# Kernel optimization log

Hardware: AMD Instinct MI355X
Metric: run time of the kernel (lower is better)

The kernel has to match this reference:

```python
import jax, jax.numpy as jnp
import numpy as np

B, SQ, SKV, D, H = 2, 2048, 2048, 1024, 16
HD = D // H  # 64
ROPE_BASE = 10000.0


def setup_inputs() -> dict:
    key = jax.random.key(0)
    ks = jax.random.split(key, 6)
    s = 1.0 / np.sqrt(D)  # keep activations well-scaled
    return {
        "x_q": jax.random.normal(ks[0], (B, SQ, D), jnp.float32),
        "x_kv": jax.random.normal(ks[1], (B, SKV, D), jnp.float32),
        "wq": jax.random.normal(ks[2], (D, D), jnp.float32) * s,
        "bq": jnp.zeros((D,), jnp.float32),
        "wk": jax.random.normal(ks[3], (D, D), jnp.float32) * s,
        "bk": jnp.zeros((D,), jnp.float32),
        "wv": jax.random.normal(ks[4], (D, D), jnp.float32) * s,
        "bv": jnp.zeros((D,), jnp.float32),
        "wo": jax.random.normal(ks[5], (D, D), jnp.float32) * s,
        "bo": jnp.zeros((D,), jnp.float32),
    }


def _rope_interleaved(x):
    # x: [B, S, H, HD]; sequential positions starting at 0 (GPT-NeoX style)
    s, hd = x.shape[1], x.shape[-1]
    dim = hd // 2
    freqs = jnp.exp(-jnp.arange(dim, dtype=x.dtype) * jnp.log(jnp.asarray(ROPE_BASE, x.dtype)) / dim)
    ang = jnp.arange(s, dtype=x.dtype)[:, None] * freqs[None, :]  # [S, dim]
    cos = jnp.cos(ang)[None, :, None, :]
    sin = jnp.sin(ang)[None, :, None, :]
    xe, xo = x[..., ::2], x[..., 1::2]
    re = xe * cos - xo * sin
    ro = xe * sin + xo * cos
    return jnp.stack([re, ro], axis=-1).reshape(x.shape)


def reference(x_q, x_kv, wq, bq, wk, bk, wv, bv, wo, bo):
    b, sq, _ = x_q.shape
    skv = x_kv.shape[1]
    q = (jnp.einsum("bsd,ed->bse", x_q, wq) + bq).reshape(b, sq, H, HD)
    k = (jnp.einsum("bsd,ed->bse", x_kv, wk) + bk).reshape(b, skv, H, HD)
    v = (jnp.einsum("bsd,ed->bse", x_kv, wv) + bv).reshape(b, skv, H, HD)
    q = _rope_interleaved(q)
    k = _rope_interleaved(k)
    scores = jnp.einsum("bqhd,bkhd->bhqk", q, k) / jnp.sqrt(jnp.asarray(HD, q.dtype))
    attn = jax.nn.softmax(scores, axis=-1)
    ctx = jnp.einsum("bhqk,bkhd->bqhd", attn, v).reshape(b, sq, D)
    return jnp.einsum("bsd,ed->bse", ctx, wo) + bo
```

## Files before the change

### kernel.cpp

```cpp
#include <hip/hip_runtime.h>
#include <cstdint>

typedef __attribute__((ext_vector_type(8))) short bf16x8;
typedef __attribute__((ext_vector_type(4))) float f32x4;
typedef __attribute__((ext_vector_type(4))) unsigned int u32x4;

#define DEV static __device__ __forceinline__

DEV unsigned short f2bf(float f) {
  unsigned int u = __builtin_bit_cast(unsigned int, f);
  u += 0x7FFFu + ((u >> 16) & 1u);
  return (unsigned short)(u >> 16);
}
#if __has_builtin(__builtin_amdgcn_cvt_pk_bf16_f32)
DEV unsigned int pkbf(float a, float b) {
  auto v = __builtin_amdgcn_cvt_pk_bf16_f32(a, b);
  return __builtin_bit_cast(unsigned int, v);
}
#else
DEV unsigned int pkbf(float a, float b) {
  return (unsigned int)f2bf(a) | ((unsigned int)f2bf(b) << 16);
}
#endif
#if __has_builtin(__builtin_amdgcn_exp2f)
#define EXP2(x) __builtin_amdgcn_exp2f(x)
#else
#define EXP2(x) exp2f(x)
#endif
DEV float bfl(unsigned int u) { return __builtin_bit_cast(float, u << 16); }
DEV float bfh(unsigned int u) { return __builtin_bit_cast(float, u & 0xFFFF0000u); }

DEV void async_copy16(const unsigned short* g, unsigned short* l) {
  __builtin_amdgcn_global_load_lds(
      (const __attribute__((address_space(1))) unsigned int*)(uintptr_t)g,
      (__attribute__((address_space(3))) unsigned int*)(uintptr_t)l,
      16, 0, 0);
}

#if __has_builtin(__builtin_amdgcn_permlane32_swap) && \
    __has_builtin(__builtin_amdgcn_permlane16_swap)
DEV void pswap(unsigned a, unsigned b, unsigned& w0, unsigned& w2, int lane) {
  (void)lane;
  auto pq = __builtin_amdgcn_permlane32_swap((int)a, (int)b, false, false);
  auto wz = __builtin_amdgcn_permlane16_swap(pq[0], pq[1], false, false);
  w0 = (unsigned)wz[0];
  w2 = (unsigned)wz[1];
}
#else
DEV void pswap(unsigned a, unsigned b, unsigned& w0, unsigned& w2, int lane) {
  int q = lane >> 4, l = lane & 15;
  int src0 = ((q & 1) << 5) + l;
  int a0 = __shfl((int)a, src0), b0 = __shfl((int)b, src0);
  int a2 = __shfl((int)a, src0 + 16), b2 = __shfl((int)b, src0 + 16);
  w0 = (unsigned)(q < 2 ? a0 : b0);
  w2 = (unsigned)(q < 2 ? a2 : b2);
}
#endif

__global__ __launch_bounds__(256) void cvt8(
    const float* __restrict__ w0, const float* __restrict__ w1,
    const float* __restrict__ w2, const float* __restrict__ w3,
    const float* __restrict__ x0, const float* __restrict__ x1,
    unsigned short* __restrict__ wsb, unsigned short* __restrict__ xb)
{
  int id = blockIdx.x * 256 + threadIdx.x;
  const float* src;
  unsigned short* dp;
  int off;
  if (id < (1 << 20)) {
    int m = id >> 18;
    off = (id & 0x3FFFF) << 2;
    src = m == 0 ? w0 : m == 1 ? w1 : m == 2 ? w2 : w3;
    dp = wsb + (((size_t)m) << 20) + off;
  } else {
    int id2 = id - (1 << 20);
    int m = id2 >> 20;
    off = (id2 & 0xFFFFF) << 2;
    src = m ? x1 : x0;
    dp = xb + (((size_t)m) << 22) + off;
  }
  float4 v = *(const float4*)(src + off);
  uint2 o;
  o.x = pkbf(v.x, v.y);
  o.y = pkbf(v.z, v.w);
  *(uint2*)dp = o;
}

__global__ __launch_bounds__(256) void gemm_qkv_bf(
    const unsigned short* __restrict__ xqb,
    const unsigned short* __restrict__ xkvb,
    const unsigned short* __restrict__ wbase,
    const float* __restrict__ bq, const float* __restrict__ bk,
    const float* __restrict__ bv,
    unsigned short* __restrict__ outq, unsigned short* __restrict__ outk,
    unsigned short* __restrict__ outvT)
{
  constexpr int K = 1024;
  __shared__ unsigned short As[128 * 32];
  __shared__ unsigned short Bs[128 * 32];
  const int z = blockIdx.z;
  const unsigned short* X = (z == 0) ? xqb : xkvb;
  const unsigned short* Wb = wbase + (((size_t)z) << 20);
  const float* bias = (z == 0) ? bq : (z == 1) ? bk : bv;

  const int tid = threadIdx.x;
  const int mBase = blockIdx.y * 128, nBase = blockIdx.x * 128;
  const int wave = tid >> 6, lane = tid & 63;
  const int quad = lane >> 4, l16 = lane & 15;
  const int wm = (wave >> 1) << 6, wn = (wave & 1) << 6;

  f32x4 acc[4][4] = {};

  for (int k0 = 0; k0 < K; k0 += 32) {
#pragma unroll
    for (int i = 0; i < 2; ++i) {
      int e = i * 2048 + tid * 8;
      int row = e >> 5, col = e & 31;
      async_copy16(X + (size_t)(mBase + row) * K + (k0 + col), &As[e]);
      async_copy16(Wb + (size_t)(nBase + row) * K + (k0 + col), &Bs[e]);
    }
    __syncthreads();
    bf16x8 af[4], bff[4];
#pragma unroll
    for (int t = 0; t < 4; ++t) {
      af[t]  = *(const bf16x8*)&As[(wm + t * 16 + l16) * 32 + quad * 8];
      bff[t] = *(const bf16x8*)&Bs[(wn + t * 16 + l16) * 32 + quad * 8];
    }
#pragma unroll
    for (int mt = 0; mt < 4; ++mt)
#pragma unroll
      for (int nt = 0; nt < 4; ++nt)
        acc[mt][nt] = __builtin_amdgcn_mfma_f32_16x16x32_bf16(af[mt], bff[nt], acc[mt][nt], 0, 0, 0);
    __syncthreads();
  }

  if (z < 2) {
    unsigned short* out = z ? outk : outq;
    const float qs = z ? 1.0f : 0.18033688011112042f;
    const int sBlk = (mBase & 2047) + wm + quad * 4;
#pragma unroll
    for (int nt = 0; nt < 4; ++nt) {
      int n = nBase + wn + nt * 16 + l16;
      float bv2 = bias[n];
      int h = n >> 6, hd = n & 63;
      int i = hd >> 1;
      int parity = n & 1;
      float f = exp2f(-(float)i * 0.4152410118609203f);
      float sf, cf;
      sincosf(f, &sf, &cf);
#pragma unroll
      for (int mt = 0; mt < 4; ++mt) {
        float ang = (float)(sBlk + mt * 16) * f;
        float s, c;
        sincosf(ang, &s, &c);
#pragma unroll
        for (int j = 0; j < 4; ++j) {
          float v = acc[mt][nt][j] + bv2;
          float pv = __shfl_xor(v, 1);
          float ce = c * qs;
          float se = (parity ? s : -s) * qs;
          float outv = v * ce + pv * se;
          int m = mBase + wm + mt * 16 + quad * 4 + j;
          int b = m >> 11, sv = m & 2047;
          out[(((size_t)(b * 16 + h) * 2048 + sv) << 6) + hd] = f2bf(outv);
          float c2 = c * cf - s * sf;
          s = s * cf + c * sf;
          c = c2;
        }
      }
    }
  } else {
#pragma unroll
    for (int nt = 0; nt < 4; ++nt) {
      int n = nBase + wn + nt * 16 + l16;
      float bv2 = bias[n];
      int h = n >> 6, hd = n & 63;
#pragma unroll
      for (int mt = 0; mt < 4; ++mt) {
        int m0 = mBase + wm + mt * 16 + quad * 4;
        int b = m0 >> 11, s = m0 & 2047;
        uint2 o;
        o.x = pkbf(acc[mt][nt][0] + bv2, acc[mt][nt][1] + bv2);
        o.y = pkbf(acc[mt][nt][2] + bv2, acc[mt][nt][3] + bv2);
        *(uint2*)&outvT[(((size_t)(b * 16 + h) * 64 + hd) << 11) + s] = o;
      }
    }
  }
}

__global__ __launch_bounds__(256) void attn_v7(
    const unsigned short* __restrict__ Qg,
    const unsigned short* __restrict__ Kg,
    const unsigned short* __restrict__ VT,
    unsigned short* __restrict__ Opart,
    float* __restrict__ lbuf)
{
  __shared__ unsigned short Ks[2][64 * 64];
  __shared__ unsigned short Vs[2][64 * 64];
  const int tid = threadIdx.x, wave = tid >> 6, lane = tid & 63;
  const int quad = lane >> 4, l16 = lane & 15;
  const int bh = blockIdx.x & 31;
  const int qt = (blockIdx.x >> 5) & 15;
  const int kvs = blockIdx.x >> 9;
  const int q0 = qt * 128 + wave * 32;
  const unsigned short* Qb = Qg + ((size_t)bh << 17);
  const unsigned short* Kb = Kg + ((size_t)bh << 17);
  const unsigned short* Vb = VT + ((size_t)bh << 17);

  const int L0 = tid, L1 = 256 + tid;
  const int r0 = L0 >> 3, r1 = L1 >> 3;
  const int c0 = ((L0 & 7) ^ (r0 & 7)) << 3;
  const int c1 = ((L1 & 7) ^ (r1 & 7)) << 3;

  bf16x8 qf[2][2];
#pragma unroll
  for (int mq = 0; mq < 2; ++mq)
#pragma unroll
    for (int kd = 0; kd < 2; ++kd)
      qf[mq][kd] = *(const bf16x8*)(Qb + (size_t)(q0 + mq * 16 + l16) * 64 + kd * 32 + quad * 8);

  f32x4 oacc[4][2] = {};
  float lacc[2] = { 0.f, 0.f };

  const int kvbeg = kvs << 10;
  const int swz = l16 & 7;

  {
    const int kv0 = kvbeg;
    async_copy16(Kb + (size_t)(kv0 + r0) * 64 + c0, &Ks[0][L0 * 8]);
    async_copy16(Kb + (size_t)(kv0 + r1) * 64 + c1, &Ks[0][L1 * 8]);
    async_copy16(Vb + (size_t)r0 * 2048 + kv0 + c0, &Vs[0][L0 * 8]);
    async_copy16(Vb + (size_t)r1 * 2048 + kv0 + c1, &Vs[0][L1 * 8]);
  }
  __syncthreads();

  for (int t = 0; t < 16; ++t) {
    const int cur = t & 1;
    if (t < 15) {
      const int kv0 = kvbeg + (t + 1) * 64;
      unsigned short* Kn = Ks[cur ^ 1];
      unsigned short* Vn = Vs[cur ^ 1];
      async_copy16(Kb + (size_t)(kv0 + r0) * 64 + c0, &Kn[L0 * 8]);
      async_copy16(Kb + (size_t)(kv0 + r1) * 64 + c1, &Kn[L1 * 8]);
      async_copy16(Vb + (size_t)r0 * 2048 + kv0 + c0, &Vn[L0 * 8]);
      async_copy16(Vb + (size_t)r1 * 2048 + kv0 + c1, &Vn[L1 * 8]);
    }
    const unsigned short* Kc = Ks[cur];
    const unsigned short* Vc = Vs[cur];

    f32x4 st[4][2] = {};
    __builtin_amdgcn_s_setprio(1);
#pragma unroll
    for (int kd = 0; kd < 2; ++kd)
#pragma unroll
      for (int tk = 0; tk < 4; ++tk) {
        bf16x8 kf = *(const bf16x8*)&Kc[(tk * 16 + l16) * 64 + (((kd * 4 + quad) ^ swz) << 3)];
#pragma unroll
        for (int mq = 0; mq < 2; ++mq)
          st[tk][mq] = __builtin_amdgcn_mfma_f32_16x16x32_bf16(kf, qf[mq][kd], st[tk][mq], 0, 0, 0);
      }
    __builtin_amdgcn_s_setprio(0);

#pragma unroll
    for (int mq = 0; mq < 2; ++mq)
#pragma unroll
      for (int tk = 0; tk < 4; ++tk)
#pragma unroll
        for (int jr = 0; jr < 4; ++jr) {
          float p = EXP2(st[tk][mq][jr]);
          st[tk][mq][jr] = p;
          lacc[mq] += p;
        }

#pragma unroll
    for (int ks = 0; ks < 2; ++ks) {
      bf16x8 pf[2];
#pragma unroll
      for (int mq = 0; mq < 2; ++mq) {
        u32x4 pw;
#pragma unroll
        for (int w = 0; w < 2; ++w) {
          unsigned a = pkbf(st[2 * ks][mq][2 * w], st[2 * ks][mq][2 * w + 1]);
          unsigned b = pkbf(st[2 * ks + 1][mq][2 * w], st[2 * ks + 1][mq][2 * w + 1]);
          unsigned w0, w2;
          pswap(a, b, w0, w2, lane);
          pw[w] = w0;
          pw[w + 2] = w2;
        }
        pf[mq] = __builtin_bit_cast(bf16x8, pw);
      }
      __builtin_amdgcn_s_setprio(1);
#pragma unroll
      for (int th = 0; th < 4; ++th) {
        bf16x8 vf = *(const bf16x8*)&Vc[(th * 16 + l16) * 64 + (((ks * 4 + quad) ^ swz) << 3)];
#pragma unroll
        for (int mq = 0; mq < 2; ++mq)
          oacc[th][mq] = __builtin_amdgcn_mfma_f32_16x16x32_bf16(vf, pf[mq], oacc[th][mq], 0, 0, 0);
      }
      __builtin_amdgcn_s_setprio(0);
    }
    __syncthreads();
  }

  const int b = bh >> 4, h = bh & 15;
  unsigned short* Od = Opart + (((size_t)kvs) << 22);
#pragma unroll
  for (int mq = 0; mq < 2; ++mq) {
    float l = lacc[mq];
    l += __shfl_xor(l, 16);
    l += __shfl_xor(l, 32);
    int s = q0 + mq * 16 + l16;
    if (quad == 0)
      lbuf[(kvs * 32 + bh) * 2048 + s] = l;
#pragma unroll
    for (int th = 0; th < 4; ++th) {
      uint2 o;
      o.x = pkbf(oacc[th][mq][0], oacc[th][mq][1]);
      o.y = pkbf(oacc[th][mq][2], oacc[th][mq][3]);
      *(uint2*)&Od[((size_t)(b * 2048 + s) << 10) + h * 64 + th * 16 + quad * 4] = o;
    }
  }
}

__global__ __launch_bounds__(256) void combine_kernel(
    const unsigned short* __restrict__ Opart, const float* __restrict__ lbuf,
    unsigned short* __restrict__ ctx)
{
  int idx = blockIdx.x * 256 + threadIdx.x;
  int m = idx >> 9;
  int c2 = idx & 511;
  int b = m >> 11, s = m & 2047;
  int h = c2 >> 5;
  int bh = b * 16 + h;
  float la = lbuf[bh * 2048 + s];
  float lb = lbuf[(32 + bh) * 2048 + s];
  float r = 1.0f / (la + lb);
  unsigned int ua = ((const unsigned int*)Opart)[idx];
  unsigned int ub = ((const unsigned int*)Opart)[(1u << 21) + idx];
  float o0 = (bfl(ua) + bfl(ub)) * r;
  float o1 = (bfh(ua) + bfh(ub)) * r;
  ((unsigned int*)ctx)[idx] = pkbf(o0, o1);
}

__global__ __launch_bounds__(256) void gemm_o_bf(
    const unsigned short* __restrict__ X,
    const unsigned short* __restrict__ Wb,
    const float* __restrict__ bias,
    float* __restrict__ out)
{
  constexpr int K = 1024;
  __shared__ unsigned short As[128 * 32];
  __shared__ unsigned short Bs[128 * 32];
  const int tid = threadIdx.x;
  const int mBase = blockIdx.y * 128, nBase = blockIdx.x * 128;
  const int wave = tid >> 6, lane = tid & 63;
  const int quad = lane >> 4, l16 = lane & 15;
  const int wm = (wave >> 1) << 6, wn = (wave & 1) << 6;

  f32x4 acc[4][4] = {};

  for (int k0 = 0; k0 < K; k0 += 32) {
#pragma unroll
    for (int i = 0; i < 2; ++i) {
      int e = i * 2048 + tid * 8;
      int row = e >> 5, col = e & 31;
      async_copy16(X + (size_t)(mBase + row) * K + (k0 + col), &As[e]);
      async_copy16(Wb + (size_t)(nBase + row) * K + (k0 + col), &Bs[e]);
    }
    __syncthreads();
    bf16x8 af[4], bff[4];
#pragma unroll
    for (int t = 0; t < 4; ++t) {
      af[t]  = *(const bf16x8*)&As[(wm + t * 16 + l16) * 32 + quad * 8];
      bff[t] = *(const bf16x8*)&Bs[(wn + t * 16 + l16) * 32 + quad * 8];
    }
#pragma unroll
    for (int mt = 0; mt < 4; ++mt)
#pragma unroll
      for (int nt = 0; nt < 4; ++nt)
        acc[mt][nt] = __builtin_amdgcn_mfma_f32_16x16x32_bf16(af[mt], bff[nt], acc[mt][nt], 0, 0, 0);
    __syncthreads();
  }

#pragma unroll
  for (int nt = 0; nt < 4; ++nt) {
    int n = nBase + wn + nt * 16 + l16;
    float bv = bias[n];
#pragma unroll
    for (int mt = 0; mt < 4; ++mt) {
#pragma unroll
      for (int j = 0; j < 4; ++j) {
        int m = mBase + wm + mt * 16 + quad * 4 + j;
        out[((size_t)m << 10) + n] = acc[mt][nt][j] + bv;
      }
    }
  }
}

extern "C" void kernel_launch(void* const* d_in, const int* in_sizes, int n_in,
                              void* d_out, int out_size, void* d_ws, size_t ws_size,
                              hipStream_t stream) {
  const float* x_q  = (const float*)d_in[0];
  const float* x_kv = (const float*)d_in[1];
  const float* wq   = (const float*)d_in[2];
  const float* bq   = (const float*)d_in[3];
  const float* wk   = (const float*)d_in[4];
  const float* bk   = (const float*)d_in[5];
  const float* wv   = (const float*)d_in[6];
  const float* bv   = (const float*)d_in[7];
  const float* wo   = (const float*)d_in[8];
  const float* bo   = (const float*)d_in[9];

  unsigned short* base = (unsigned short*)d_ws;
  unsigned short* ob   = (unsigned short*)d_out;

  unsigned short* wob  = base + (3u << 20);
  unsigned short* k    = base + (4u << 20);
  unsigned short* vT   = base + (8u << 20);
  unsigned short* q    = base + (12u << 20);
  unsigned short* ctx  = q;
  float*          lbuf = (float*)d_ws;
  unsigned short* xqb  = ob;
  unsigned short* xkvb = ob + (4u << 20);
  unsigned short* Opart = ob;
  float* out = (float*)d_out;

  cvt8<<<12288, 256, 0, stream>>>(wq, wk, wv, wo, x_q, x_kv, base, ob);
  gemm_qkv_bf<<<dim3(8, 32, 3), 256, 0, stream>>>(xqb, xkvb, base,
                                                  bq, bk, bv, q, k, vT);
  attn_v7<<<1024, 256, 0, stream>>>(q, k, vT, Opart, lbuf);
  combine_kernel<<<8192, 256, 0, stream>>>(Opart, lbuf, ctx);
  gemm_o_bf<<<dim3(8, 32), 256, 0, stream>>>(ctx, wob, bo, out);
}
```

Before: 246.6 us.

## Double-buffer and swizzle LDS in projection GEMMs, halve output GEMM M-tile

Both bf16 GEMMs now use two LDS buffers, so the async global-to-LDS copy of the next K-slice is issued while MFMAs run on the current one. The LDS layout gets an XOR swizzle on 16-byte chunks to reduce bank conflicts on the fragment reads. The output-projection GEMM's M-tile drops from 128 to 64, doubling its grid to 512 blocks for better CU occupancy. The cost is a larger LDS footprint per block and less reuse per block in the output GEMM. The trailing __syncthreads appears to remain the only barrier, which the buffer alternation should make sufficient.

```diff
diff --git a/kernel.cpp b/kernel.cpp
--- a/kernel.cpp
+++ b/kernel.cpp
@@ -96,8 +96,8 @@
     unsigned short* __restrict__ outvT)
 {
   constexpr int K = 1024;
-  __shared__ unsigned short As[128 * 32];
-  __shared__ unsigned short Bs[128 * 32];
+  __shared__ unsigned short As[2][128 * 32];
+  __shared__ unsigned short Bs[2][128 * 32];
   const int z = blockIdx.z;
   const unsigned short* X = (z == 0) ? xqb : xkvb;
   const unsigned short* Wb = wbase + (((size_t)z) << 20);
@@ -109,22 +109,33 @@
   const int quad = lane >> 4, l16 = lane & 15;
   const int wm = (wave >> 1) << 6, wn = (wave & 1) << 6;
 
+  const int L0 = tid, L1 = 256 + tid;
+  const int r0 = L0 >> 2, c0 = ((L0 & 3) ^ (r0 & 3)) << 3;
+  const int r1 = L1 >> 2, c1 = ((L1 & 3) ^ (r1 & 3)) << 3;
+
   f32x4 acc[4][4] = {};
 
-  for (int k0 = 0; k0 < K; k0 += 32) {
-#pragma unroll
-    for (int i = 0; i < 2; ++i) {
-      int e = i * 2048 + tid * 8;
-      int row = e >> 5, col = e & 31;
-      async_copy16(X + (size_t)(mBase + row) * K + (k0 + col), &As[e]);
-      async_copy16(Wb + (size_t)(nBase + row) * K + (k0 + col), &Bs[e]);
-    }
-    __syncthreads();
+  async_copy16(X + (size_t)(mBase + r0) * K + c0, &As[0][L0 * 8]);
+  async_copy16(X + (size_t)(mBase + r1) * K + c1, &As[0][L1 * 8]);
+  async_copy16(Wb + (size_t)(nBase + r0) * K + c0, &Bs[0][L0 * 8]);
+  async_copy16(Wb + (size_t)(nBase + r1) * K + c1, &Bs[0][L1 * 8]);
+  __syncthreads();
+
+  const int sw = (quad ^ (l16 & 3)) << 3;
+  for (int it = 0; it < 32; ++it) {
+    const int cur = it & 1;
+    if (it < 31) {
+      const int k0 = (it + 1) * 32;
+      async_copy16(X + (size_t)(mBase + r0) * K + k0 + c0, &As[cur ^ 1][L0 * 8]);
+      async_copy16(X + (size_t)(mBase + r1) * K + k0 + c1, &As[cur ^ 1][L1 * 8]);
+      async_copy16(Wb + (size_t)(nBase + r0) * K + k0 + c0, &Bs[cur ^ 1][L0 * 8]);
+      async_copy16(Wb + (size_t)(nBase + r1) * K + k0 + c1, &Bs[cur ^ 1][L1 * 8]);
+    }
     bf16x8 af[4], bff[4];
 #pragma unroll
     for (int t = 0; t < 4; ++t) {
-      af[t]  = *(const bf16x8*)&As[(wm + t * 16 + l16) * 32 + quad * 8];
-      bff[t] = *(const bf16x8*)&Bs[(wn + t * 16 + l16) * 32 + quad * 8];
+      af[t]  = *(const bf16x8*)&As[cur][(wm + t * 16 + l16) * 32 + sw];
+      bff[t] = *(const bf16x8*)&Bs[cur][(wn + t * 16 + l16) * 32 + sw];
     }
 #pragma unroll
     for (int mt = 0; mt < 4; ++mt)
@@ -349,33 +360,42 @@
     float* __restrict__ out)
 {
   constexpr int K = 1024;
-  __shared__ unsigned short As[128 * 32];
-  __shared__ unsigned short Bs[128 * 32];
+  __shared__ unsigned short As[2][64 * 32];
+  __shared__ unsigned short Bs[2][128 * 32];
   const int tid = threadIdx.x;
-  const int mBase = blockIdx.y * 128, nBase = blockIdx.x * 128;
+  const int mBase = blockIdx.y * 64, nBase = blockIdx.x * 128;
   const int wave = tid >> 6, lane = tid & 63;
   const int quad = lane >> 4, l16 = lane & 15;
-  const int wm = (wave >> 1) << 6, wn = (wave & 1) << 6;
-
-  f32x4 acc[4][4] = {};
-
-  for (int k0 = 0; k0 < K; k0 += 32) {
-#pragma unroll
-    for (int i = 0; i < 2; ++i) {
-      int e = i * 2048 + tid * 8;
-      int row = e >> 5, col = e & 31;
-      async_copy16(X + (size_t)(mBase + row) * K + (k0 + col), &As[e]);
-      async_copy16(Wb + (size_t)(nBase + row) * K + (k0 + col), &Bs[e]);
-    }
-    __syncthreads();
-    bf16x8 af[4], bff[4];
-#pragma unroll
-    for (int t = 0; t < 4; ++t) {
-      af[t]  = *(const bf16x8*)&As[(wm + t * 16 + l16) * 32 + quad * 8];
-      bff[t] = *(const bf16x8*)&Bs[(wn + t * 16 + l16) * 32 + quad * 8];
-    }
-#pragma unroll
-    for (int mt = 0; mt < 4; ++mt)
+  const int wm = (wave >> 1) << 5, wn = (wave & 1) << 6;
+
+  const int La = tid, ra = La >> 2, ca = ((La & 3) ^ (ra & 3)) << 3;
+  const int Lb1 = 256 + tid, rb1 = Lb1 >> 2, cb1 = ((Lb1 & 3) ^ (rb1 & 3)) << 3;
+
+  f32x4 acc[2][4] = {};
+
+  async_copy16(X + (size_t)(mBase + ra) * K + ca, &As[0][La * 8]);
+  async_copy16(Wb + (size_t)(nBase + ra) * K + ca, &Bs[0][La * 8]);
+  async_copy16(Wb + (size_t)(nBase + rb1) * K + cb1, &Bs[0][Lb1 * 8]);
+  __syncthreads();
+
+  const int sw = (quad ^ (l16 & 3)) << 3;
+  for (int it = 0; it < 32; ++it) {
+    const int cur = it & 1;
+    if (it < 31) {
+      const int k0 = (it + 1) * 32;
+      async_copy16(X + (size_t)(mBase + ra) * K + k0 + ca, &As[cur ^ 1][La * 8]);
+      async_copy16(Wb + (size_t)(nBase + ra) * K + k0 + ca, &Bs[cur ^ 1][La * 8]);
+      async_copy16(Wb + (size_t)(nBase + rb1) * K + k0 + cb1, &Bs[cur ^ 1][Lb1 * 8]);
+    }
+    bf16x8 af[2], bff[4];
+#pragma unroll
+    for (int t = 0; t < 2; ++t)
+      af[t] = *(const bf16x8*)&As[cur][(wm + t * 16 + l16) * 32 + sw];
+#pragma unroll
+    for (int t = 0; t < 4; ++t)
+      bff[t] = *(const bf16x8*)&Bs[cur][(wn + t * 16 + l16) * 32 + sw];
+#pragma unroll
+    for (int mt = 0; mt < 2; ++mt)
 #pragma unroll
       for (int nt = 0; nt < 4; ++nt)
         acc[mt][nt] = __builtin_amdgcn_mfma_f32_16x16x32_bf16(af[mt], bff[nt], acc[mt][nt], 0, 0, 0);
@@ -387,7 +407,7 @@
     int n = nBase + wn + nt * 16 + l16;
     float bv = bias[n];
 #pragma unroll
-    for (int mt = 0; mt < 4; ++mt) {
+    for (int mt = 0; mt < 2; ++mt) {
 #pragma unroll
       for (int j = 0; j < 4; ++j) {
         int m = mBase + wm + mt * 16 + quad * 4 + j;
@@ -430,5 +450,5 @@
                                                   bq, bk, bv, q, k, vT);
   attn_v7<<<1024, 256, 0, stream>>>(q, k, vT, Opart, lbuf);
   combine_kernel<<<8192, 256, 0, stream>>>(Opart, lbuf, ctx);
-  gemm_o_bf<<<dim3(8, 32), 256, 0, stream>>>(ctx, wob, bo, out);
-}
+  gemm_o_bf<<<dim3(8, 64), 256, 0, stream>>>(ctx, wob, bo, out);
+}
```

After: 240.8 us. -2.3%, faster.
